# Performance work log

Measured on AMD Instinct MI355X. Metric: run time of the kernel, lower is better.

Reference implementation:

```python
import jax, jax.numpy as jnp
import numpy as np

N = 50000
E = 800000
D_IN = 64
D_OUT = 64
D_EDGE = 16


def setup_inputs() -> dict:
    key = jax.random.key(0)
    ks = jax.random.split(key, 10)
    x = jax.random.normal(ks[0], (N, D_IN), dtype=jnp.float32)
    edge_index = jax.random.randint(ks[1], (2, E), 0, N, dtype=jnp.int64)
    edge_attr = jax.random.normal(ks[2], (E, D_EDGE), dtype=jnp.float32)
    s = 1.0 / np.sqrt(D_EDGE)
    We = jax.random.uniform(ks[3], (D_EDGE, D_IN), minval=-s, maxval=s, dtype=jnp.float32)
    be = jax.random.uniform(ks[4], (D_IN,), minval=-s, maxval=s, dtype=jnp.float32)
    s1 = 1.0 / np.sqrt(D_IN)
    W1 = jax.random.uniform(ks[5], (D_IN, D_OUT), minval=-s1, maxval=s1, dtype=jnp.float32)
    b1 = jax.random.uniform(ks[6], (D_OUT,), minval=-s1, maxval=s1, dtype=jnp.float32)
    s2 = 1.0 / np.sqrt(D_OUT)
    W2 = jax.random.uniform(ks[7], (D_OUT, D_OUT), minval=-s2, maxval=s2, dtype=jnp.float32)
    b2 = jax.random.uniform(ks[8], (D_OUT,), minval=-s2, maxval=s2, dtype=jnp.float32)
    return {"x": x, "edge_index": edge_index, "edge_attr": edge_attr,
            "We": We, "be": be, "W1": W1, "b1": b1, "W2": W2, "b2": b2}


def reference(x, edge_index, edge_attr, We, be, W1, b1, W2, b2):
    src = edge_index[0]  # message source j
    dst = edge_index[1]  # aggregation target i (PyG source_to_target flow)
    # per-edge message: relu(x_j + lin_edge(edge_attr))
    msg = jax.nn.relu(x[src] + edge_attr @ We + be)  # [E, D_IN]
    # scatter-sum aggregation at target nodes
    agg = jax.ops.segment_sum(msg, dst, num_segments=N)  # [N, D_IN]
    eps = 0.0  # GINEConv default, train_eps=False
    h = (1.0 + eps) * x + agg
    # mlp: Linear -> ReLU -> Linear (dropout p=0.0 -> identity)
    out = jax.nn.relu(h @ W1 + b1) @ W2 + b2
    return out
```

## Files before the change

### kernel.cpp

```cpp
#include <hip/hip_runtime.h>
#include <hip/hip_bf16.h>

#define NN 50000
#define EE 800000

__device__ __forceinline__ float bflo(unsigned u) { return __uint_as_float(u << 16); }
__device__ __forceinline__ float bfhi(unsigned u) { return __uint_as_float(u & 0xffff0000u); }

__global__ void detect_dtype(const unsigned* __restrict__ xw, int* __restrict__ flag) {
    if (threadIdx.x == 0 && blockIdx.x == 0) {
        int cnt = 0;
        for (int i = 0; i < 64; i++) {
            unsigned e = (xw[i] >> 7) & 0xFFu;
            if (e >= 100u && e <= 140u) cnt++;
        }
        *flag = (cnt >= 32) ? 1 : 0;
    }
}

template <bool BF16>
__device__ __forceinline__ void edge_body(
    const void* __restrict__ xv, const int* __restrict__ ei,
    const void* __restrict__ eav, const void* __restrict__ Wev,
    const void* __restrict__ bev, float* __restrict__ agg)
{
    const int tid = threadIdx.x;
    const int d   = tid & 63;
    const int sub = tid >> 6;

    const int oddor = ei[1] | ei[3] | ei[5] | ei[7] | ei[9] | ei[11] | ei[13] | ei[15];
    const bool idx64 = (oddor == 0);
    const long long* __restrict__ ei64 = (const long long*)ei;

    float we[16];
    float bed;
    if constexpr (BF16) {
        const __hip_bfloat16* We = (const __hip_bfloat16*)Wev;
        const __hip_bfloat16* be = (const __hip_bfloat16*)bev;
#pragma unroll
        for (int k = 0; k < 16; k++) we[k] = __bfloat162float(We[k * 64 + d]);
        bed = __bfloat162float(be[d]);
    } else {
        const float* We = (const float*)Wev;
        const float* be = (const float*)bev;
#pragma unroll
        for (int k = 0; k < 16; k++) we[k] = We[k * 64 + d];
        bed = be[d];
    }

    const int stride = gridDim.x * 4;
    for (int e = blockIdx.x * 4 + sub; e < EE; e += stride) {
        int src, dst;
        if (idx64) { src = (int)ei64[e]; dst = (int)ei64[EE + e]; }
        else       { src = ei[e];        dst = ei[EE + e]; }

        float a[16];
        if constexpr (BF16) {
            const uint4* row = (const uint4*)((const __hip_bfloat16*)eav + (size_t)e * 16);
            const uint4 p0 = row[0];
            const uint4 p1 = row[1];
            a[0]=bflo(p0.x); a[1]=bfhi(p0.x); a[2]=bflo(p0.y); a[3]=bfhi(p0.y);
            a[4]=bflo(p0.z); a[5]=bfhi(p0.z); a[6]=bflo(p0.w); a[7]=bfhi(p0.w);
            a[8]=bflo(p1.x); a[9]=bfhi(p1.x); a[10]=bflo(p1.y); a[11]=bfhi(p1.y);
            a[12]=bflo(p1.z); a[13]=bfhi(p1.z); a[14]=bflo(p1.w); a[15]=bfhi(p1.w);
        } else {
            const float4* row = (const float4*)((const float*)eav + (size_t)e * 16);
            const float4 q0 = row[0], q1 = row[1], q2 = row[2], q3 = row[3];
            a[0]=q0.x; a[1]=q0.y; a[2]=q0.z; a[3]=q0.w;
            a[4]=q1.x; a[5]=q1.y; a[6]=q1.z; a[7]=q1.w;
            a[8]=q2.x; a[9]=q2.y; a[10]=q2.z; a[11]=q2.w;
            a[12]=q3.x; a[13]=q3.y; a[14]=q3.z; a[15]=q3.w;
        }

        float acc = bed;
#pragma unroll
        for (int k = 0; k < 16; k++) acc = fmaf(a[k], we[k], acc);

        float xs;
        if constexpr (BF16) xs = __bfloat162float(((const __hip_bfloat16*)xv)[(size_t)src * 64 + d]);
        else                xs = ((const float*)xv)[(size_t)src * 64 + d];

        float msg = fmaxf(acc + xs, 0.0f);
        unsafeAtomicAdd(&agg[(size_t)dst * 64 + d], msg);
    }
}

__global__ __launch_bounds__(256) void edge_agg_kernel(
    const void* x, const int* ei, const void* ea,
    const void* We, const void* be, float* agg, const int* flag)
{
    if (*flag) edge_body<true>(x, ei, ea, We, be, agg);
    else       edge_body<false>(x, ei, ea, We, be, agg);
}

template <bool BF16>
__device__ __forceinline__ void mlp_body(
    const void* __restrict__ xv, const float* __restrict__ agg,
    const void* __restrict__ W1v, const void* __restrict__ b1v,
    const void* __restrict__ W2v, const void* __restrict__ b2v,
    void* __restrict__ outv)
{
    __shared__ float sh[4][64];
    __shared__ float st[4][64];
    const int tid = threadIdx.x;
    const int d   = tid & 63;
    const int w   = tid >> 6;

    float w1c[64], w2c[64], b1d, b2d;
    if constexpr (BF16) {
        const __hip_bfloat16* W1 = (const __hip_bfloat16*)W1v;
        const __hip_bfloat16* W2 = (const __hip_bfloat16*)W2v;
#pragma unroll
        for (int k = 0; k < 64; k++) {
            w1c[k] = __bfloat162float(W1[k * 64 + d]);
            w2c[k] = __bfloat162float(W2[k * 64 + d]);
        }
        b1d = __bfloat162float(((const __hip_bfloat16*)b1v)[d]);
        b2d = __bfloat162float(((const __hip_bfloat16*)b2v)[d]);
    } else {
        const float* W1 = (const float*)W1v;
        const float* W2 = (const float*)W2v;
#pragma unroll
        for (int k = 0; k < 64; k++) {
            w1c[k] = W1[k * 64 + d];
            w2c[k] = W2[k * 64 + d];
        }
        b1d = ((const float*)b1v)[d];
        b2d = ((const float*)b2v)[d];
    }

    const int stride = gridDim.x * 4;
    const int iters  = (NN + stride - 1) / stride;
    int node = blockIdx.x * 4 + w;
    for (int it = 0; it < iters; it++, node += stride) {
        const bool valid = node < NN;
        if (valid) {
            float xs;
            if constexpr (BF16) xs = __bfloat162float(((const __hip_bfloat16*)xv)[(size_t)node * 64 + d]);
            else                xs = ((const float*)xv)[(size_t)node * 64 + d];
            sh[w][d] = xs + agg[(size_t)node * 64 + d];
        }
        __syncthreads();

        float t = b1d;
        const float4* hv = (const float4*)sh[w];
#pragma unroll
        for (int k = 0; k < 16; k++) {
            const float4 hq = hv[k];
            t = fmaf(hq.x, w1c[4 * k],     t);
            t = fmaf(hq.y, w1c[4 * k + 1], t);
            t = fmaf(hq.z, w1c[4 * k + 2], t);
            t = fmaf(hq.w, w1c[4 * k + 3], t);
        }
        t = fmaxf(t, 0.0f);
        st[w][d] = t;
        __syncthreads();

        float o = b2d;
        const float4* tv = (const float4*)st[w];
#pragma unroll
        for (int k = 0; k < 16; k++) {
            const float4 tq = tv[k];
            o = fmaf(tq.x, w2c[4 * k],     o);
            o = fmaf(tq.y, w2c[4 * k + 1], o);
            o = fmaf(tq.z, w2c[4 * k + 2], o);
            o = fmaf(tq.w, w2c[4 * k + 3], o);
        }
        if (valid) {
            if constexpr (BF16) ((__hip_bfloat16*)outv)[(size_t)node * 64 + d] = __float2bfloat16(o);
            else                ((float*)outv)[(size_t)node * 64 + d] = o;
        }
    }
}

__global__ __launch_bounds__(256) void mlp_kernel(
    const void* x, const float* agg,
    const void* W1, const void* b1, const void* W2, const void* b2,
    void* out, const int* flag)
{
    if (*flag) mlp_body<true>(x, agg, W1, b1, W2, b2, out);
    else       mlp_body<false>(x, agg, W1, b1, W2, b2, out);
}

extern "C" void kernel_launch(void* const* d_in, const int* in_sizes, int n_in,
                              void* d_out, int out_size, void* d_ws, size_t ws_size,
                              hipStream_t stream) {
    const void* x          = d_in[0];
    const int*  edge_index = (const int*)d_in[1];
    const void* edge_attr  = d_in[2];
    const void* We         = d_in[3];
    const void* be         = d_in[4];
    const void* W1         = d_in[5];
    const void* b1         = d_in[6];
    const void* W2         = d_in[7];
    const void* b2         = d_in[8];

    float* agg  = (float*)d_ws;
    int*   flag = (int*)((char*)d_ws + (size_t)NN * 64 * sizeof(float));

    hipMemsetAsync(agg, 0, (size_t)NN * 64 * sizeof(float), stream);
    hipLaunchKernelGGL(detect_dtype, dim3(1), dim3(64), 0, stream,
                       (const unsigned*)x, flag);
    hipLaunchKernelGGL(edge_agg_kernel, dim3(4096), dim3(256), 0, stream,
                       x, edge_index, edge_attr, We, be, agg, flag);
    hipLaunchKernelGGL(mlp_kernel, dim3(2048), dim3(256), 0, stream,
                       x, agg, W1, b1, W2, b2, d_out, flag);
}
```

Measured before the change: 324.6 us.

## Batch four edges per wave in edge kernel and drop MLP block barriers

The edge aggregation loop now handles four consecutive edges per wavefront per iteration. It loads their indices together (int4 when indices are 32-bit) and issues the four x-row gathers before the edge-linear math, so more memory requests are in flight. The MLP kernel drops its __syncthreads barriers, because each 64-wide wavefront only reads its own shared-memory row. The dtype detection uses a wave ballot in place of a serial single-thread loop. Without barriers, correctness depends on intra-wavefront LDS ordering, and the four-edge batching assumes EE is divisible by 4.

```diff
diff --git a/kernel.cpp b/kernel.cpp
--- a/kernel.cpp
+++ b/kernel.cpp
@@ -8,14 +8,41 @@
 __device__ __forceinline__ float bfhi(unsigned u) { return __uint_as_float(u & 0xffff0000u); }
 
 __global__ void detect_dtype(const unsigned* __restrict__ xw, int* __restrict__ flag) {
-    if (threadIdx.x == 0 && blockIdx.x == 0) {
-        int cnt = 0;
-        for (int i = 0; i < 64; i++) {
-            unsigned e = (xw[i] >> 7) & 0xFFu;
-            if (e >= 100u && e <= 140u) cnt++;
-        }
-        *flag = (cnt >= 32) ? 1 : 0;
-    }
+    const int t = threadIdx.x;
+    unsigned e = (xw[t] >> 7) & 0xFFu;
+    unsigned long long m = __ballot(e >= 100u && e <= 140u);
+    if (t == 0) *flag = (__popcll(m) >= 32) ? 1 : 0;
+}
+
+template <bool BF16>
+__device__ __forceinline__ float edge_lin(const void* __restrict__ eav, int e,
+                                          const float* __restrict__ we, float bed) {
+    float acc = bed;
+    if constexpr (BF16) {
+        const uint4* row = (const uint4*)((const __hip_bfloat16*)eav + (size_t)e * 16);
+        const uint4 p0 = row[0];
+        const uint4 p1 = row[1];
+        acc = fmaf(bflo(p0.x), we[0],  acc); acc = fmaf(bfhi(p0.x), we[1],  acc);
+        acc = fmaf(bflo(p0.y), we[2],  acc); acc = fmaf(bfhi(p0.y), we[3],  acc);
+        acc = fmaf(bflo(p0.z), we[4],  acc); acc = fmaf(bfhi(p0.z), we[5],  acc);
+        acc = fmaf(bflo(p0.w), we[6],  acc); acc = fmaf(bfhi(p0.w), we[7],  acc);
+        acc = fmaf(bflo(p1.x), we[8],  acc); acc = fmaf(bfhi(p1.x), we[9],  acc);
+        acc = fmaf(bflo(p1.y), we[10], acc); acc = fmaf(bfhi(p1.y), we[11], acc);
+        acc = fmaf(bflo(p1.z), we[12], acc); acc = fmaf(bfhi(p1.z), we[13], acc);
+        acc = fmaf(bflo(p1.w), we[14], acc); acc = fmaf(bfhi(p1.w), we[15], acc);
+    } else {
+        const float4* row = (const float4*)((const float*)eav + (size_t)e * 16);
+        const float4 q0 = row[0], q1 = row[1], q2 = row[2], q3 = row[3];
+        acc = fmaf(q0.x, we[0],  acc); acc = fmaf(q0.y, we[1],  acc);
+        acc = fmaf(q0.z, we[2],  acc); acc = fmaf(q0.w, we[3],  acc);
+        acc = fmaf(q1.x, we[4],  acc); acc = fmaf(q1.y, we[5],  acc);
+        acc = fmaf(q1.z, we[6],  acc); acc = fmaf(q1.w, we[7],  acc);
+        acc = fmaf(q2.x, we[8],  acc); acc = fmaf(q2.y, we[9],  acc);
+        acc = fmaf(q2.z, we[10], acc); acc = fmaf(q2.w, we[11], acc);
+        acc = fmaf(q3.x, we[12], acc); acc = fmaf(q3.y, we[13], acc);
+        acc = fmaf(q3.z, we[14], acc); acc = fmaf(q3.w, we[15], acc);
+    }
+    return acc;
 }
 
 template <bool BF16>
@@ -36,52 +63,51 @@
     float bed;
     if constexpr (BF16) {
         const __hip_bfloat16* We = (const __hip_bfloat16*)Wev;
-        const __hip_bfloat16* be = (const __hip_bfloat16*)bev;
 #pragma unroll
         for (int k = 0; k < 16; k++) we[k] = __bfloat162float(We[k * 64 + d]);
-        bed = __bfloat162float(be[d]);
+        bed = __bfloat162float(((const __hip_bfloat16*)bev)[d]);
     } else {
         const float* We = (const float*)Wev;
-        const float* be = (const float*)bev;
 #pragma unroll
         for (int k = 0; k < 16; k++) we[k] = We[k * 64 + d];
-        bed = be[d];
-    }
-
-    const int stride = gridDim.x * 4;
-    for (int e = blockIdx.x * 4 + sub; e < EE; e += stride) {
-        int src, dst;
-        if (idx64) { src = (int)ei64[e]; dst = (int)ei64[EE + e]; }
-        else       { src = ei[e];        dst = ei[EE + e]; }
-
-        float a[16];
-        if constexpr (BF16) {
-            const uint4* row = (const uint4*)((const __hip_bfloat16*)eav + (size_t)e * 16);
-            const uint4 p0 = row[0];
-            const uint4 p1 = row[1];
-            a[0]=bflo(p0.x); a[1]=bfhi(p0.x); a[2]=bflo(p0.y); a[3]=bfhi(p0.y);
-            a[4]=bflo(p0.z); a[5]=bfhi(p0.z); a[6]=bflo(p0.w); a[7]=bfhi(p0.w);
-            a[8]=bflo(p1.x); a[9]=bfhi(p1.x); a[10]=bflo(p1.y); a[11]=bfhi(p1.y);
-            a[12]=bflo(p1.z); a[13]=bfhi(p1.z); a[14]=bflo(p1.w); a[15]=bfhi(p1.w);
+        bed = ((const float*)bev)[d];
+    }
+
+    const int wid = blockIdx.x * 4 + sub;
+    const int nw  = gridDim.x * 4;
+    for (int e0 = wid * 4; e0 < EE; e0 += nw * 4) {
+        int src[4], dst[4];
+        if (idx64) {
+#pragma unroll
+            for (int i = 0; i < 4; i++) {
+                src[i] = (int)ei64[e0 + i];
+                dst[i] = (int)ei64[EE + e0 + i];
+            }
         } else {
-            const float4* row = (const float4*)((const float*)eav + (size_t)e * 16);
-            const float4 q0 = row[0], q1 = row[1], q2 = row[2], q3 = row[3];
-            a[0]=q0.x; a[1]=q0.y; a[2]=q0.z; a[3]=q0.w;
-            a[4]=q1.x; a[5]=q1.y; a[6]=q1.z; a[7]=q1.w;
-            a[8]=q2.x; a[9]=q2.y; a[10]=q2.z; a[11]=q2.w;
-            a[12]=q3.x; a[13]=q3.y; a[14]=q3.z; a[15]=q3.w;
-        }
-
-        float acc = bed;
-#pragma unroll
-        for (int k = 0; k < 16; k++) acc = fmaf(a[k], we[k], acc);
-
-        float xs;
-        if constexpr (BF16) xs = __bfloat162float(((const __hip_bfloat16*)xv)[(size_t)src * 64 + d]);
-        else                xs = ((const float*)xv)[(size_t)src * 64 + d];
-
-        float msg = fmaxf(acc + xs, 0.0f);
-        unsafeAtomicAdd(&agg[(size_t)dst * 64 + d], msg);
+            const int4 s4 = *(const int4*)(ei + e0);
+            const int4 d4 = *(const int4*)(ei + EE + e0);
+            src[0] = s4.x; src[1] = s4.y; src[2] = s4.z; src[3] = s4.w;
+            dst[0] = d4.x; dst[1] = d4.y; dst[2] = d4.z; dst[3] = d4.w;
+        }
+
+        float xs[4];
+#pragma unroll
+        for (int i = 0; i < 4; i++) {
+            if constexpr (BF16)
+                xs[i] = __bfloat162float(((const __hip_bfloat16*)xv)[(size_t)src[i] * 64 + d]);
+            else
+                xs[i] = ((const float*)xv)[(size_t)src[i] * 64 + d];
+        }
+
+        float acc[4];
+#pragma unroll
+        for (int i = 0; i < 4; i++) acc[i] = edge_lin<BF16>(eav, e0 + i, we, bed);
+
+#pragma unroll
+        for (int i = 0; i < 4; i++) {
+            float msg = fmaxf(acc[i] + xs[i], 0.0f);
+            unsafeAtomicAdd(&agg[(size_t)dst[i] * 64 + d], msg);
+        }
     }
 }
 
@@ -130,17 +156,11 @@
     }
 
     const int stride = gridDim.x * 4;
-    const int iters  = (NN + stride - 1) / stride;
-    int node = blockIdx.x * 4 + w;
-    for (int it = 0; it < iters; it++, node += stride) {
-        const bool valid = node < NN;
-        if (valid) {
-            float xs;
-            if constexpr (BF16) xs = __bfloat162float(((const __hip_bfloat16*)xv)[(size_t)node * 64 + d]);
-            else                xs = ((const float*)xv)[(size_t)node * 64 + d];
-            sh[w][d] = xs + agg[(size_t)node * 64 + d];
-        }
-        __syncthreads();
+    for (int node = blockIdx.x * 4 + w; node < NN; node += stride) {
+        float xs;
+        if constexpr (BF16) xs = __bfloat162float(((const __hip_bfloat16*)xv)[(size_t)node * 64 + d]);
+        else                xs = ((const float*)xv)[(size_t)node * 64 + d];
+        sh[w][d] = xs + agg[(size_t)node * 64 + d];
 
         float t = b1d;
         const float4* hv = (const float4*)sh[w];
@@ -154,7 +174,6 @@
         }
         t = fmaxf(t, 0.0f);
         st[w][d] = t;
-        __syncthreads();
 
         float o = b2d;
         const float4* tv = (const float4*)st[w];
@@ -166,10 +185,8 @@
             o = fmaf(tq.z, w2c[4 * k + 2], o);
             o = fmaf(tq.w, w2c[4 * k + 3], o);
         }
-        if (valid) {
-            if constexpr (BF16) ((__hip_bfloat16*)outv)[(size_t)node * 64 + d] = __float2bfloat16(o);
-            else                ((float*)outv)[(size_t)node * 64 + d] = o;
-        }
+        if constexpr (BF16) ((__hip_bfloat16*)outv)[(size_t)node * 64 + d] = __float2bfloat16(o);
+        else                ((float*)outv)[(size_t)node * 64 + d] = o;
     }
 }
 
```

New measurement: 309.2 us. 4.7% less time.
